# Kernel optimization log

Hardware: AMD Instinct MI355X
Metric: run time of the kernel (lower is better)

## Reference

```python
import jax, jax.numpy as jnp
import numpy as np

NEG_INF = -1e9
LRELU_SLOPE = 0.2

B, C, FIN, FOUT = 8, 2048, 128, 64


def setup_inputs() -> dict:
    key = jax.random.key(0)
    k1, k2, k3, k4 = jax.random.split(key, 4)
    H = jax.random.normal(k1, (B, C, FIN), dtype=jnp.float32)
    A = jax.random.randint(k2, (B, C, C), 0, 2, dtype=jnp.int32)
    W = jax.random.normal(k3, (FIN, FOUT), dtype=jnp.float32)
    a = jax.random.normal(k4, (2 * FOUT,), dtype=jnp.float32)
    return {"H": H, "A": A, "W": W, "a": a}


def reference(H, A, W, a):
    # Wh: [B, C, F]
    Wh = jnp.einsum("bcf,fo->bco", H, W)
    F = Wh.shape[-1]
    a1, a2 = a[:F], a[F:]
    # e_ij = a . concat(Wh_i, Wh_j) = (Wh_i . a1) + (Wh_j . a2)
    # -> never materialize the (B,C,C,2F) concat tensor; same math.
    s1 = jnp.einsum("bcf,f->bc", Wh, a1)  # [B, C] contribution of node i
    s2 = jnp.einsum("bcf,f->bc", Wh, a2)  # [B, C] contribution of node j
    e = jax.nn.leaky_relu(s1[:, :, None] + s2[:, None, :], LRELU_SLOPE)  # [B,C,C]
    mask = (A > 0) | jnp.eye(A.shape[-1], dtype=bool)[None]
    e = jnp.where(mask, e, NEG_INF)
    alpha = jax.nn.softmax(e, axis=-1)
    # dropout omitted (eval mode) for a deterministic correctness baseline
    out = jax.nn.relu(jnp.einsum("bij,bjf->bif", alpha, Wh))
    return out
```

## Files before the change

### kernel.cpp

```cpp
#include <hip/hip_runtime.h>

#define NB 8
#define NC 2048
#define KIN 128
#define NF 64

#define WTSTRIDE 136
#define RSTRIDE 68
#define MOFF 60.0f

typedef float floatx4_t __attribute__((ext_vector_type(4)));
typedef __bf16 bf16x8_t __attribute__((ext_vector_type(8)));
typedef unsigned short ushort8_t __attribute__((ext_vector_type(8)));

static __device__ __forceinline__ unsigned short f2bf(float f) {
  union { float f; unsigned int u; } v; v.f = f;
  unsigned int u = v.u;
  u += 0x7FFFu + ((u >> 16) & 1u);
  return (unsigned short)(u >> 16);
}

static __device__ __forceinline__ float lrelu(float x) {
  return fmaxf(x, 0.2f * x);
}

__global__ __launch_bounds__(256, 2) void k1_prep(
    const float* __restrict__ H, const float* __restrict__ W,
    const float* __restrict__ avec,
    float* __restrict__ s1g, float* __restrict__ s2g,
    unsigned short* __restrict__ WhT)
{
  __shared__ unsigned short WTsh[NF * WTSTRIDE];
  __shared__ float w1sh[KIN];
  __shared__ float w2sh[KIN];

  const int t = threadIdx.x;
  const int b = blockIdx.x >> 5;
  const int c0 = (blockIdx.x & 31) * 64;

  for (int i = t; i < KIN * NF; i += 256) {
    int k = i >> 6, f = i & 63;
    WTsh[f * WTSTRIDE + k] = f2bf(W[i]);
  }
  if (t < KIN) {
    float acc1 = 0.f, acc2 = 0.f;
    const float* wr = W + t * NF;
#pragma unroll
    for (int f = 0; f < NF; ++f) {
      float wv = wr[f];
      acc1 += wv * avec[f];
      acc2 += wv * avec[NF + f];
    }
    w1sh[t] = acc1;
    w2sh[t] = acc2;
  }
  __syncthreads();

  {
    const int r = t >> 2;
    const int qq = t & 3;
    const float* hp = H + (size_t)(b * NC + c0 + r) * KIN + qq * 32;
    const float* w1p = w1sh + qq * 32;
    const float* w2p = w2sh + qq * 32;
    float p1 = 0.f, p2 = 0.f;
#pragma unroll
    for (int j = 0; j < 8; ++j) {
      float4 h = *(const float4*)(hp + j * 4);
      float4 u1 = *(const float4*)(w1p + j * 4);
      float4 u2 = *(const float4*)(w2p + j * 4);
      p1 += h.x * u1.x + h.y * u1.y + h.z * u1.z + h.w * u1.w;
      p2 += h.x * u2.x + h.y * u2.y + h.z * u2.z + h.w * u2.w;
    }
    p1 += __shfl_xor(p1, 1); p2 += __shfl_xor(p2, 1);
    p1 += __shfl_xor(p1, 2); p2 += __shfl_xor(p2, 2);
    if (qq == 0) {
      s1g[b * NC + c0 + r] = p1;
      s2g[b * NC + c0 + r] = p2;
    }
  }

  const int wave = t >> 6;
  const int lane = t & 63;
  const int m = lane & 15;
  const int q = lane >> 4;
  floatx4_t acc[4];
#pragma unroll
  for (int mt = 0; mt < 4; ++mt) acc[mt] = (floatx4_t){0.f, 0.f, 0.f, 0.f};

  const float* hb = H + (size_t)(b * NC + c0 + wave * 16 + m) * KIN;
#pragma unroll
  for (int kt = 0; kt < 4; ++kt) {
    const int kbase = kt * 32 + q * 8;
    float4 h0 = *(const float4*)(hb + kbase);
    float4 h1 = *(const float4*)(hb + kbase + 4);
    ushort8_t bu;
    bu[0] = f2bf(h0.x); bu[1] = f2bf(h0.y); bu[2] = f2bf(h0.z); bu[3] = f2bf(h0.w);
    bu[4] = f2bf(h1.x); bu[5] = f2bf(h1.y); bu[6] = f2bf(h1.z); bu[7] = f2bf(h1.w);
    bf16x8_t bf = __builtin_bit_cast(bf16x8_t, bu);
#pragma unroll
    for (int mt = 0; mt < 4; ++mt) {
      ushort8_t au = *(const ushort8_t*)(WTsh + (mt * 16 + m) * WTSTRIDE + kbase);
      bf16x8_t af = __builtin_bit_cast(bf16x8_t, au);
      acc[mt] = __builtin_amdgcn_mfma_f32_16x16x32_bf16(af, bf, acc[mt], 0, 0, 0);
    }
  }
#pragma unroll
  for (int mt = 0; mt < 4; ++mt) {
#pragma unroll
    for (int i2 = 0; i2 < 4; ++i2) {
      const int f = mt * 16 + q * 4 + i2;
      WhT[(size_t)(b * NF + f) * NC + c0 + wave * 16 + m] = f2bf(acc[mt][i2]);
    }
  }
}

__global__ __launch_bounds__(256, 2) void k2_attn(
    const int* __restrict__ A, const float* __restrict__ s1g,
    const float* __restrict__ s2g, const unsigned short* __restrict__ WhT,
    float* __restrict__ out)
{
  __shared__ float s2_sh[NC];
  __shared__ float s1_sh[16];
  __shared__ float wmax_sh[4];
  __shared__ float red_sh[4 * 16 * RSTRIDE];
  __shared__ float lsum_sh[4 * 16];

  const int t = threadIdx.x;
  const int b = blockIdx.x >> 7;
  const int i0 = (blockIdx.x & 127) * 16;
  const int wave = t >> 6;
  const int lane = t & 63;

  float lmax;
  {
    const float* sp = s2g + b * NC;
    float4 v0 = *(const float4*)(sp + t * 4);
    float4 v1 = *(const float4*)(sp + 1024 + t * 4);
    *(float4*)(s2_sh + t * 4) = v0;
    *(float4*)(s2_sh + 1024 + t * 4) = v1;
    lmax = fmaxf(fmaxf(fmaxf(v0.x, v0.y), fmaxf(v0.z, v0.w)),
                 fmaxf(fmaxf(v1.x, v1.y), fmaxf(v1.z, v1.w)));
#pragma unroll
    for (int off = 1; off < 64; off <<= 1)
      lmax = fmaxf(lmax, __shfl_xor(lmax, off));
    if (lane == 0) wmax_sh[wave] = lmax;
  }
  if (t < 16) s1_sh[t] = s1g[b * NC + i0 + t];
  __syncthreads();

  const float s2max =
      fmaxf(fmaxf(wmax_sh[0], wmax_sh[1]), fmaxf(wmax_sh[2], wmax_sh[3]));

  const int m = lane & 15;
  const int q = lane >> 4;
  const int gi = i0 + m;
  const float s1m = s1_sh[m];
  const float mm = lrelu(s1m + s2max) - MOFF;
  const int* Ap = A + ((size_t)b * NC + gi) * NC;
  const unsigned short* whb = WhT + (size_t)b * NF * NC;

  ushort8_t ou;
  {
    const unsigned short ov = (m == 0) ? (unsigned short)0x3F80 : (unsigned short)0;
#pragma unroll
    for (int idx = 0; idx < 8; ++idx) ou[idx] = ov;
  }
  const bf16x8_t onesf = __builtin_bit_cast(bf16x8_t, ou);

  floatx4_t acc[4], accl;
#pragma unroll
  for (int nt = 0; nt < 4; ++nt) acc[nt] = (floatx4_t){0.f, 0.f, 0.f, 0.f};
  accl = (floatx4_t){0.f, 0.f, 0.f, 0.f};

  const int ktBeg = wave * 16, ktEnd = wave * 16 + 16;
  int4 pa0, pa1;
  {
    const int* ap = Ap + ktBeg * 32 + q * 8;
    pa0 = *(const int4*)ap;
    pa1 = *(const int4*)(ap + 4);
  }

  for (int kt = ktBeg; kt < ktEnd; ++kt) {
    const int4 a0 = pa0, a1 = pa1;
    if (kt + 1 < ktEnd) {
      const int* ap = Ap + (kt + 1) * 32 + q * 8;
      pa0 = *(const int4*)ap;
      pa1 = *(const int4*)(ap + 4);
    }
    const int jq = kt * 32 + q * 8;
    float4 s0 = *(const float4*)(s2_sh + jq);
    float4 s1v = *(const float4*)(s2_sh + jq + 4);
    const float sv[8] = {s0.x, s0.y, s0.z, s0.w, s1v.x, s1v.y, s1v.z, s1v.w};
    const int av[8] = {a0.x, a0.y, a0.z, a0.w, a1.x, a1.y, a1.z, a1.w};
    ushort8_t au;
#pragma unroll
    for (int idx = 0; idx < 8; ++idx) {
      float x = s1m + sv[idx];
      float p = __expf(lrelu(x) - mm);
      bool keep = (av[idx] > 0) || (jq + idx == gi);
      au[idx] = keep ? f2bf(p) : (unsigned short)0;
    }
    const bf16x8_t af = __builtin_bit_cast(bf16x8_t, au);
#pragma unroll
    for (int nt = 0; nt < 4; ++nt) {
      ushort8_t bu = *(const ushort8_t*)(whb + (size_t)(nt * 16 + m) * NC + jq);
      bf16x8_t bf = __builtin_bit_cast(bf16x8_t, bu);
      acc[nt] = __builtin_amdgcn_mfma_f32_16x16x32_bf16(af, bf, acc[nt], 0, 0, 0);
    }
    accl = __builtin_amdgcn_mfma_f32_16x16x32_bf16(af, onesf, accl, 0, 0, 0);
  }

#pragma unroll
  for (int nt = 0; nt < 4; ++nt) {
#pragma unroll
    for (int i2 = 0; i2 < 4; ++i2) {
      red_sh[wave * (16 * RSTRIDE) + (q * 4 + i2) * RSTRIDE + nt * 16 + m] =
          acc[nt][i2];
    }
  }
  if (m == 0) {
#pragma unroll
    for (int i2 = 0; i2 < 4; ++i2)
      lsum_sh[wave * 16 + q * 4 + i2] = accl[i2];
  }
  __syncthreads();

  {
    const int row = t >> 4;
    const int f0 = (t & 15) * 4;
    float4 v = {0.f, 0.f, 0.f, 0.f};
    float ls = 0.f;
#pragma unroll
    for (int w = 0; w < 4; ++w) {
      const float* rp = red_sh + w * (16 * RSTRIDE) + row * RSTRIDE + f0;
      float4 vv = *(const float4*)rp;
      v.x += vv.x; v.y += vv.y; v.z += vv.z; v.w += vv.w;
      ls += lsum_sh[w * 16 + row];
    }
    const float inv = 1.0f / ls;
    float4 o;
    o.x = fmaxf(v.x * inv, 0.f);
    o.y = fmaxf(v.y * inv, 0.f);
    o.z = fmaxf(v.z * inv, 0.f);
    o.w = fmaxf(v.w * inv, 0.f);
    *(float4*)(out + (size_t)(b * NC + i0 + row) * NF + f0) = o;
  }
}

extern "C" void kernel_launch(void* const* d_in, const int* in_sizes, int n_in,
                              void* d_out, int out_size, void* d_ws, size_t ws_size,
                              hipStream_t stream) {
  const float* H = (const float*)d_in[0];
  const int* A = (const int*)d_in[1];
  const float* W = (const float*)d_in[2];
  const float* avec = (const float*)d_in[3];
  float* out = (float*)d_out;

  char* ws = (char*)d_ws;
  unsigned short* WhT = (unsigned short*)ws;
  float* s1 = (float*)(ws + (size_t)NB * NF * NC * 2);
  float* s2 = s1 + NB * NC;

  k1_prep<<<dim3(NB * (NC / 64)), dim3(256), 0, stream>>>(H, W, avec, s1, s2, WhT);
  k2_attn<<<dim3(NB * (NC / 16)), dim3(256), 0, stream>>>(A, s1, s2, WhT, out);
}
```

Before: 227.0 us.

## Retile prep kernel, deepen A prefetch, and cheapen exp/bf16 packing in attention

The prep kernel now covers 16 nodes per block instead of 64, giving four times as many blocks, with each wave computing one 16-wide feature slice. The attention kernel prefetches A two tiles ahead with a double buffer, issues the WhT loads before the exp work, and computes exp with exp2f plus a folded log2e FMA. It also packs bf16 by truncation through v_perm instead of round-to-nearest conversion. Launch bounds rise to 4 blocks per CU, which may cap registers, and truncation slightly changes numerics.

```diff
diff --git a/kernel.cpp b/kernel.cpp
--- a/kernel.cpp
+++ b/kernel.cpp
@@ -8,6 +8,7 @@
 #define WTSTRIDE 136
 #define RSTRIDE 68
 #define MOFF 60.0f
+#define LOG2E 1.44269504088896340736f
 
 typedef float floatx4_t __attribute__((ext_vector_type(4)));
 typedef __bf16 bf16x8_t __attribute__((ext_vector_type(8)));
@@ -24,7 +25,7 @@
   return fmaxf(x, 0.2f * x);
 }
 
-__global__ __launch_bounds__(256, 2) void k1_prep(
+__global__ __launch_bounds__(256, 4) void k1_prep(
     const float* __restrict__ H, const float* __restrict__ W,
     const float* __restrict__ avec,
     float* __restrict__ s1g, float* __restrict__ s2g,
@@ -35,8 +36,8 @@
   __shared__ float w2sh[KIN];
 
   const int t = threadIdx.x;
-  const int b = blockIdx.x >> 5;
-  const int c0 = (blockIdx.x & 31) * 64;
+  const int b = blockIdx.x >> 7;
+  const int c0 = (blockIdx.x & 127) * 16;
 
   for (int i = t; i < KIN * NF; i += 256) {
     int k = i >> 6, f = i & 63;
@@ -57,23 +58,25 @@
   __syncthreads();
 
   {
-    const int r = t >> 2;
-    const int qq = t & 3;
-    const float* hp = H + (size_t)(b * NC + c0 + r) * KIN + qq * 32;
-    const float* w1p = w1sh + qq * 32;
-    const float* w2p = w2sh + qq * 32;
-    float p1 = 0.f, p2 = 0.f;
-#pragma unroll
-    for (int j = 0; j < 8; ++j) {
-      float4 h = *(const float4*)(hp + j * 4);
-      float4 u1 = *(const float4*)(w1p + j * 4);
-      float4 u2 = *(const float4*)(w2p + j * 4);
-      p1 += h.x * u1.x + h.y * u1.y + h.z * u1.z + h.w * u1.w;
-      p2 += h.x * u2.x + h.y * u2.y + h.z * u2.z + h.w * u2.w;
-    }
-    p1 += __shfl_xor(p1, 1); p2 += __shfl_xor(p2, 1);
-    p1 += __shfl_xor(p1, 2); p2 += __shfl_xor(p2, 2);
-    if (qq == 0) {
+    const int r = t >> 4;
+    const int x = t & 15;
+    const float* hp = H + (size_t)(b * NC + c0 + r) * KIN + x * 8;
+    float4 h0 = *(const float4*)(hp);
+    float4 h1 = *(const float4*)(hp + 4);
+    float4 u10 = *(const float4*)(w1sh + x * 8);
+    float4 u11 = *(const float4*)(w1sh + x * 8 + 4);
+    float4 u20 = *(const float4*)(w2sh + x * 8);
+    float4 u21 = *(const float4*)(w2sh + x * 8 + 4);
+    float p1 = h0.x * u10.x + h0.y * u10.y + h0.z * u10.z + h0.w * u10.w
+             + h1.x * u11.x + h1.y * u11.y + h1.z * u11.z + h1.w * u11.w;
+    float p2 = h0.x * u20.x + h0.y * u20.y + h0.z * u20.z + h0.w * u20.w
+             + h1.x * u21.x + h1.y * u21.y + h1.z * u21.z + h1.w * u21.w;
+#pragma unroll
+    for (int off = 1; off < 16; off <<= 1) {
+      p1 += __shfl_xor(p1, off);
+      p2 += __shfl_xor(p2, off);
+    }
+    if (x == 0) {
       s1g[b * NC + c0 + r] = p1;
       s2g[b * NC + c0 + r] = p2;
     }
@@ -83,11 +86,9 @@
   const int lane = t & 63;
   const int m = lane & 15;
   const int q = lane >> 4;
-  floatx4_t acc[4];
-#pragma unroll
-  for (int mt = 0; mt < 4; ++mt) acc[mt] = (floatx4_t){0.f, 0.f, 0.f, 0.f};
-
-  const float* hb = H + (size_t)(b * NC + c0 + wave * 16 + m) * KIN;
+  floatx4_t acc = (floatx4_t){0.f, 0.f, 0.f, 0.f};
+
+  const float* hb = H + (size_t)(b * NC + c0 + m) * KIN;
 #pragma unroll
   for (int kt = 0; kt < 4; ++kt) {
     const int kbase = kt * 32 + q * 8;
@@ -97,24 +98,18 @@
     bu[0] = f2bf(h0.x); bu[1] = f2bf(h0.y); bu[2] = f2bf(h0.z); bu[3] = f2bf(h0.w);
     bu[4] = f2bf(h1.x); bu[5] = f2bf(h1.y); bu[6] = f2bf(h1.z); bu[7] = f2bf(h1.w);
     bf16x8_t bf = __builtin_bit_cast(bf16x8_t, bu);
-#pragma unroll
-    for (int mt = 0; mt < 4; ++mt) {
-      ushort8_t au = *(const ushort8_t*)(WTsh + (mt * 16 + m) * WTSTRIDE + kbase);
-      bf16x8_t af = __builtin_bit_cast(bf16x8_t, au);
-      acc[mt] = __builtin_amdgcn_mfma_f32_16x16x32_bf16(af, bf, acc[mt], 0, 0, 0);
-    }
-  }
-#pragma unroll
-  for (int mt = 0; mt < 4; ++mt) {
-#pragma unroll
-    for (int i2 = 0; i2 < 4; ++i2) {
-      const int f = mt * 16 + q * 4 + i2;
-      WhT[(size_t)(b * NF + f) * NC + c0 + wave * 16 + m] = f2bf(acc[mt][i2]);
-    }
-  }
-}
-
-__global__ __launch_bounds__(256, 2) void k2_attn(
+    ushort8_t au = *(const ushort8_t*)(WTsh + (wave * 16 + m) * WTSTRIDE + kbase);
+    bf16x8_t af = __builtin_bit_cast(bf16x8_t, au);
+    acc = __builtin_amdgcn_mfma_f32_16x16x32_bf16(af, bf, acc, 0, 0, 0);
+  }
+#pragma unroll
+  for (int i2 = 0; i2 < 4; ++i2) {
+    const int f = wave * 16 + q * 4 + i2;
+    WhT[(size_t)(b * NF + f) * NC + c0 + m] = f2bf(acc[i2]);
+  }
+}
+
+__global__ __launch_bounds__(256, 4) void k2_attn(
     const int* __restrict__ A, const float* __restrict__ s1g,
     const float* __restrict__ s2g, const unsigned short* __restrict__ WhT,
     float* __restrict__ out)
@@ -155,7 +150,7 @@
   const int q = lane >> 4;
   const int gi = i0 + m;
   const float s1m = s1_sh[m];
-  const float mm = lrelu(s1m + s2max) - MOFF;
+  const float mmL = (lrelu(s1m + s2max) - MOFF) * LOG2E;
   const int* Ap = A + ((size_t)b * NC + gi) * NC;
   const unsigned short* whb = WhT + (size_t)b * NF * NC;
 
@@ -172,39 +167,57 @@
   for (int nt = 0; nt < 4; ++nt) acc[nt] = (floatx4_t){0.f, 0.f, 0.f, 0.f};
   accl = (floatx4_t){0.f, 0.f, 0.f, 0.f};
 
-  const int ktBeg = wave * 16, ktEnd = wave * 16 + 16;
-  int4 pa0, pa1;
-  {
-    const int* ap = Ap + ktBeg * 32 + q * 8;
-    pa0 = *(const int4*)ap;
-    pa1 = *(const int4*)(ap + 4);
-  }
-
-  for (int kt = ktBeg; kt < ktEnd; ++kt) {
-    const int4 a0 = pa0, a1 = pa1;
-    if (kt + 1 < ktEnd) {
-      const int* ap = Ap + (kt + 1) * 32 + q * 8;
-      pa0 = *(const int4*)ap;
-      pa1 = *(const int4*)(ap + 4);
-    }
+  const int ktBeg = wave * 16;
+  int4 abuf[2][2];
+  {
+    const int* ap0 = Ap + ktBeg * 32 + q * 8;
+    abuf[0][0] = *(const int4*)ap0;
+    abuf[0][1] = *(const int4*)(ap0 + 4);
+    const int* ap1 = ap0 + 32;
+    abuf[1][0] = *(const int4*)ap1;
+    abuf[1][1] = *(const int4*)(ap1 + 4);
+  }
+
+#pragma unroll 2
+  for (int kk = 0; kk < 16; ++kk) {
+    const int kt = ktBeg + kk;
     const int jq = kt * 32 + q * 8;
+    const int cur = kk & 1;
+    const int4 a0 = abuf[cur][0];
+    const int4 a1 = abuf[cur][1];
+    if (kk + 2 < 16) {
+      const int* ap = Ap + (kt + 2) * 32 + q * 8;
+      abuf[cur][0] = *(const int4*)ap;
+      abuf[cur][1] = *(const int4*)(ap + 4);
+    }
+    ushort8_t whc[4];
+#pragma unroll
+    for (int nt = 0; nt < 4; ++nt)
+      whc[nt] = *(const ushort8_t*)(whb + (size_t)(nt * 16 + m) * NC + jq);
+
     float4 s0 = *(const float4*)(s2_sh + jq);
     float4 s1v = *(const float4*)(s2_sh + jq + 4);
     const float sv[8] = {s0.x, s0.y, s0.z, s0.w, s1v.x, s1v.y, s1v.z, s1v.w};
     const int av[8] = {a0.x, a0.y, a0.z, a0.w, a1.x, a1.y, a1.z, a1.w};
-    ushort8_t au;
+    const int d = gi - jq;
+    unsigned int pu[8];
 #pragma unroll
     for (int idx = 0; idx < 8; ++idx) {
       float x = s1m + sv[idx];
-      float p = __expf(lrelu(x) - mm);
-      bool keep = (av[idx] > 0) || (jq + idx == gi);
-      au[idx] = keep ? f2bf(p) : (unsigned short)0;
-    }
-    const bf16x8_t af = __builtin_bit_cast(bf16x8_t, au);
+      float p = __builtin_amdgcn_exp2f(fmaf(lrelu(x), LOG2E, -mmL));
+      bool keep = (av[idx] > 0) || (d == idx);
+      p = keep ? p : 0.0f;
+      pu[idx] = __builtin_bit_cast(unsigned int, p);
+    }
+    uint4 pk;
+    pk.x = __builtin_amdgcn_perm(pu[1], pu[0], 0x07060302u);
+    pk.y = __builtin_amdgcn_perm(pu[3], pu[2], 0x07060302u);
+    pk.z = __builtin_amdgcn_perm(pu[5], pu[4], 0x07060302u);
+    pk.w = __builtin_amdgcn_perm(pu[7], pu[6], 0x07060302u);
+    const bf16x8_t af = __builtin_bit_cast(bf16x8_t, pk);
 #pragma unroll
     for (int nt = 0; nt < 4; ++nt) {
-      ushort8_t bu = *(const ushort8_t*)(whb + (size_t)(nt * 16 + m) * NC + jq);
-      bf16x8_t bf = __builtin_bit_cast(bf16x8_t, bu);
+      bf16x8_t bf = __builtin_bit_cast(bf16x8_t, whc[nt]);
       acc[nt] = __builtin_amdgcn_mfma_f32_16x16x32_bf16(af, bf, acc[nt], 0, 0, 0);
     }
     accl = __builtin_amdgcn_mfma_f32_16x16x32_bf16(af, onesf, accl, 0, 0, 0);
@@ -261,6 +274,6 @@
   float* s1 = (float*)(ws + (size_t)NB * NF * NC * 2);
   float* s2 = s1 + NB * NC;
 
-  k1_prep<<<dim3(NB * (NC / 64)), dim3(256), 0, stream>>>(H, W, avec, s1, s2, WhT);
+  k1_prep<<<dim3(NB * (NC / 16)), dim3(256), 0, stream>>>(H, W, avec, s1, s2, WhT);
   k2_attn<<<dim3(NB * (NC / 16)), dim3(256), 0, stream>>>(A, s1, s2, WhT, out);
 }
```

New measurement: 232.2 us. 2.3% more time.
